# Performance work log

Hardware: AMD Instinct MI355X
Metric: run time of the kernel (lower is better)

The kernel has to match this reference:

```python
import jax, jax.numpy as jnp
import numpy as np

X = 2048      # hidden units per layer
Z = 4         # number of hidden layers
IN = 512      # input_dim
OUT = 256     # output_dim
B = 64        # batch
T = 128       # time steps
KEEP = 0.7    # Bernoulli keep prob y
RES = [0, 0, 1, 2]  # residual_in (first two unused by the branch structure)
NFUN = 5      # number of candidate transfer functions


def setup_inputs() -> dict:
    key = jax.random.key(0)
    ks = jax.random.split(key, 12)
    f32 = jnp.float32
    x = jax.random.normal(ks[0], (B, T, IN), f32)
    W_in = jax.random.normal(ks[1], (X, IN), f32) * jax.random.bernoulli(ks[2], KEEP, (X, IN)).astype(f32)
    b_in = jax.random.normal(ks[3], (X,), f32)
    W_h = jax.random.normal(ks[4], (Z, X, 2 * X), f32)
    # lateral inhibition block: hidden layer 1, second-half columns, zero diagonal
    lat = jax.random.normal(ks[5], (X, X), f32) * (1.0 - jnp.eye(X, dtype=f32))
    W_h = W_h.at[1, :, X:].set(lat)
    W_h = W_h * jax.random.bernoulli(ks[6], KEEP, (Z, X, 2 * X)).astype(f32)
    b_h = jax.random.normal(ks[7], (Z, X), f32)
    W_out = jax.random.normal(ks[8], (OUT, X), f32) * jax.random.bernoulli(ks[9], KEEP, (OUT, X)).astype(f32)
    b_out = jax.random.normal(ks[10], (OUT,), f32)
    act_ids = jax.random.randint(ks[11], (Z + 1, X), 0, NFUN)
    out_act_ids = jax.random.randint(jax.random.fold_in(key, 99), (OUT,), 0, NFUN)
    return dict(x=x, W_in=W_in, b_in=b_in, W_h=W_h, b_h=b_h,
                W_out=W_out, b_out=b_out, act_ids=act_ids, out_act_ids=out_act_ids)


def _rand_act(h, ids):
    # per-column random nonlinearity: ids [D] in {relu, sigmoid, tanh, leaky_relu(0.1), selu}
    stk = jnp.stack([
        jax.nn.relu(h),
        jax.nn.sigmoid(h),
        jnp.tanh(h),
        jnp.where(h >= 0, h, 0.1 * h),
        jax.nn.selu(h),
    ], axis=0)  # [5, B, D]
    oh = jax.nn.one_hot(ids, NFUN, dtype=h.dtype)  # [D, 5]
    return jnp.einsum('fbd,df->bd', stk, oh)


def _l2norm(v, eps=1e-12):
    # torch F.normalize along dim=1
    return v / jnp.maximum(jnp.linalg.norm(v, axis=1, keepdims=True), eps)


def reference(x, W_in, b_in, W_h, b_h, W_out, b_out, act_ids, out_act_ids):
    batch = x.shape[0]

    def step(carry, xt):
        bp, li = carry  # backprojection state, lateral inhibition state
        h0 = _rand_act(xt @ W_in.T + b_in, act_ids[0])
        h1 = _rand_act(jnp.concatenate([h0, bp], axis=-1) @ W_h[0].T + b_h[0], act_ids[1])
        h2 = _rand_act(jnp.concatenate([h1, li], axis=-1) @ W_h[1].T + b_h[1], act_ids[2])
        li_new = _l2norm(h2)
        outs = [h0, h1, h2]
        for i in range(2, Z):
            hin = jnp.concatenate([outs[i], outs[RES[i]]], axis=-1)
            outs.append(_rand_act(hin @ W_h[i].T + b_h[i], act_ids[i + 1]))
        bp_new = _l2norm(outs[-1])
        yt = _rand_act(outs[-1] @ W_out.T + b_out, out_act_ids)
        return (bp_new, li_new), yt

    init = (jnp.zeros((batch, X), x.dtype), jnp.zeros((batch, X), x.dtype))
    _, ys = jax.lax.scan(step, init, jnp.swapaxes(x, 0, 1))  # scan over time
    return jnp.swapaxes(ys, 0, 1)  # [B, T, OUT]
```

## Files before the change

### kernel.cpp

```cpp
#include <hip/hip_runtime.h>
#include <stdint.h>


typedef __bf16 bf16;
typedef __attribute__((ext_vector_type(8))) __bf16 bf16x8;
typedef __attribute__((ext_vector_type(4))) float f32x4;

#define BATCH 64
#define TSTEPS 128
#define INDIM 512
#define XDIM 2048
#define OUTDIM 256
#define SLOTE ((size_t)BATCH * XDIM)

__device__ __forceinline__ float apply_act(float h, int id) {
  switch (id) {
    case 0: return fmaxf(h, 0.0f);
    case 1: return 1.0f / (1.0f + __expf(-h));
    case 2: return tanhf(h);
    case 3: return h >= 0.0f ? h : 0.1f * h;
    default: {
      const float sc = 1.0507009873554805f;
      const float al = 1.6732632423543772f;
      return h > 0.0f ? sc * h : sc * al * (__expf(h) - 1.0f);
    }
  }
}

template <bool SCALE_A2, bool EMIT_SS>
__global__ __launch_bounds__(512, 2) void step_gemm8(
    const bf16* __restrict__ A1, const bf16* __restrict__ A2,
    const bf16* __restrict__ W, const float* __restrict__ bias,
    const int* __restrict__ acts, const float* __restrict__ ss_in,
    float* __restrict__ ss_out, bf16* __restrict__ outb) {
  const int tid = threadIdx.x;
  const int lane = tid & 63;
  const int w = tid >> 6;
  const int l15 = lane & 15;
  const int kb8 = (lane >> 4) * 8;
  const int nblk = blockIdx.x * 16;
  const int mrow = blockIdx.y * 32;

  const bf16* As = (w >= 4) ? A2 : A1;
  const int koff = (w & 3) * 512;
  const int wk = w * 512;

  const bf16* ap0 = As + (size_t)(mrow + l15) * 2048 + koff + kb8;
  const bf16* ap1 = ap0 + 16 * 2048;
  const bf16* bpw = W + (size_t)(nblk + l15) * 4096 + wk + kb8;

  f32x4 acc0 = {0.f, 0.f, 0.f, 0.f};
  f32x4 acc1 = {0.f, 0.f, 0.f, 0.f};
#pragma unroll
  for (int k = 0; k < 512; k += 32) {
    bf16x8 a0 = *(const bf16x8*)(ap0 + k);
    bf16x8 a1 = *(const bf16x8*)(ap1 + k);
    bf16x8 b  = *(const bf16x8*)(bpw + k);
    acc0 = __builtin_amdgcn_mfma_f32_16x16x32_bf16(a0, b, acc0, 0, 0, 0);
    acc1 = __builtin_amdgcn_mfma_f32_16x16x32_bf16(a1, b, acc1, 0, 0, 0);
  }

  __shared__ float red[8][32][17];
  const int q4 = lane >> 4;
#pragma unroll
  for (int r = 0; r < 4; r++) red[w][q4 * 4 + r][l15] = acc0[r];
#pragma unroll
  for (int r = 0; r < 4; r++) red[w][16 + q4 * 4 + r][l15] = acc1[r];
  __syncthreads();

  if (tid < 256) {
    const int row = tid >> 3;
    const int c0 = (tid & 7) * 2;
    const int rg = mrow + row;

    float scale = 1.0f;
    if (SCALE_A2) scale = 1.0f / fmaxf(sqrtf(ss_in[rg]), 1e-12f);

    float v[2];
#pragma unroll
    for (int j = 0; j < 2; j++) {
      int c = c0 + j;
      float lo = red[0][row][c] + red[1][row][c] + red[2][row][c] + red[3][row][c];
      float hi = red[4][row][c] + red[5][row][c] + red[6][row][c] + red[7][row][c];
      float pre = (SCALE_A2 ? (lo + scale * hi) : (lo + hi)) + bias[nblk + c];
      v[j] = apply_act(pre, acts[nblk + c]);
    }
    if (EMIT_SS) {
      float ss = v[0] * v[0] + v[1] * v[1];
      ss += __shfl_xor(ss, 1);
      ss += __shfl_xor(ss, 2);
      ss += __shfl_xor(ss, 4);
      if ((tid & 7) == 0) atomicAdd(ss_out + rg, ss);
    }
    union { bf16 b2[2]; uint32_t u; } pk;
    pk.b2[0] = (bf16)v[0];
    pk.b2[1] = (bf16)v[1];
    *(uint32_t*)(outb + (size_t)rg * XDIM + nblk + c0) = pk.u;
  }
}

__global__ __launch_bounds__(256) void h0_gemm(
    const bf16* __restrict__ A, const bf16* __restrict__ W,
    const float* __restrict__ bias, const int* __restrict__ acts,
    bf16* __restrict__ outp) {
  const int tid = threadIdx.x;
  const int lane = tid & 63;
  const int wv = tid >> 6;
  const int wm = (wv & 1) * 32;
  const int wn = (wv >> 1) * 64;
  const int nblk = blockIdx.x * 128;
  const int mblk = blockIdx.y * 64;
  const int l15 = lane & 15;
  const int kb8 = (lane >> 4) * 8;

  f32x4 acc[2][4];
  const f32x4 zero = {0.f, 0.f, 0.f, 0.f};
#pragma unroll
  for (int i = 0; i < 2; i++)
#pragma unroll
    for (int j = 0; j < 4; j++) acc[i][j] = zero;

  for (int kt = 0; kt < INDIM; kt += 32) {
    bf16x8 a[2], b[4];
#pragma unroll
    for (int mt = 0; mt < 2; mt++) {
      int m = mblk + wm + mt * 16 + l15;
      a[mt] = *(const bf16x8*)(A + (size_t)m * INDIM + kt + kb8);
    }
#pragma unroll
    for (int nt = 0; nt < 4; nt++) {
      int n = nblk + wn + nt * 16 + l15;
      b[nt] = *(const bf16x8*)(W + (size_t)n * INDIM + kt + kb8);
    }
#pragma unroll
    for (int mt = 0; mt < 2; mt++)
#pragma unroll
      for (int nt = 0; nt < 4; nt++)
        acc[mt][nt] = __builtin_amdgcn_mfma_f32_16x16x32_bf16(a[mt], b[nt], acc[mt][nt], 0, 0, 0);
  }

#pragma unroll
  for (int mt = 0; mt < 2; mt++) {
#pragma unroll
    for (int nt = 0; nt < 4; nt++) {
      int n = nblk + wn + nt * 16 + l15;
      float bv = bias[n];
      int aid = acts[n];
#pragma unroll
      for (int rr = 0; rr < 4; rr++) {
        int m = wm + mt * 16 + (lane >> 4) * 4 + rr;
        float v = apply_act(acc[mt][nt][rr] + bv, aid);
        int rowg = mblk + m;
        int bb = rowg >> 7;
        int tt = rowg & 127;
        outp[((size_t)tt * BATCH + bb) * XDIM + n] = (bf16)v;
      }
    }
  }
}

__global__ __launch_bounds__(256) void ybat_gemm(
    const bf16* __restrict__ extra, const bf16* __restrict__ h0,
    const bf16* __restrict__ Wout, const float* __restrict__ bout,
    const int* __restrict__ oact, float* __restrict__ out) {
  const int t = blockIdx.y;
  const int s = t + 1;
  const bf16* A = (s < 2) ? (extra + (size_t)s * SLOTE)
                          : (h0 + (size_t)(s - 2) * SLOTE);
  const int tid = threadIdx.x;
  const int lane = tid & 63;
  const int wv = tid >> 6;
  const int wm = (wv & 1) * 32;
  const int wn = (wv >> 1) * 64;
  const int nblk = blockIdx.x * 128;
  const int l15 = lane & 15;
  const int kb8 = (lane >> 4) * 8;

  f32x4 acc[2][4];
  const f32x4 zero = {0.f, 0.f, 0.f, 0.f};
#pragma unroll
  for (int i = 0; i < 2; i++)
#pragma unroll
    for (int j = 0; j < 4; j++) acc[i][j] = zero;

  for (int kt = 0; kt < XDIM; kt += 32) {
    bf16x8 a[2], b[4];
#pragma unroll
    for (int mt = 0; mt < 2; mt++) {
      int m = wm + mt * 16 + l15;
      a[mt] = *(const bf16x8*)(A + (size_t)m * XDIM + kt + kb8);
    }
#pragma unroll
    for (int nt = 0; nt < 4; nt++) {
      int n = nblk + wn + nt * 16 + l15;
      b[nt] = *(const bf16x8*)(Wout + (size_t)n * XDIM + kt + kb8);
    }
#pragma unroll
    for (int mt = 0; mt < 2; mt++)
#pragma unroll
      for (int nt = 0; nt < 4; nt++)
        acc[mt][nt] = __builtin_amdgcn_mfma_f32_16x16x32_bf16(a[mt], b[nt], acc[mt][nt], 0, 0, 0);
  }

#pragma unroll
  for (int mt = 0; mt < 2; mt++) {
#pragma unroll
    for (int nt = 0; nt < 4; nt++) {
      int n = nblk + wn + nt * 16 + l15;
      float bv = bout[n];
      int aid = oact[n];
#pragma unroll
      for (int rr = 0; rr < 4; rr++) {
        int b = wm + mt * 16 + (lane >> 4) * 4 + rr;
        float v = apply_act(acc[mt][nt][rr] + bv, aid);
        out[((size_t)b * TSTEPS + t) * OUTDIM + n] = v;
      }
    }
  }
}

__global__ __launch_bounds__(256) void cvt_bf16(
    const float* __restrict__ in, bf16* __restrict__ out, int n4) {
  int i = blockIdx.x * 256 + threadIdx.x;
  if (i < n4) {
    float4 v = ((const float4*)in)[i];
    union { bf16 b[4]; unsigned long long u; } pk;
    pk.b[0] = (bf16)v.x;
    pk.b[1] = (bf16)v.y;
    pk.b[2] = (bf16)v.z;
    pk.b[3] = (bf16)v.w;
    ((unsigned long long*)out)[i] = pk.u;
  }
}

__global__ __launch_bounds__(256) void zero32(uint32_t* __restrict__ p, int n) {
  int i = blockIdx.x * 256 + threadIdx.x;
  if (i < n) p[i] = 0u;
}

extern "C" void kernel_launch(void* const* d_in, const int* in_sizes, int n_in,
                              void* d_out, int out_size, void* d_ws, size_t ws_size,
                              hipStream_t stream) {
  const float* x     = (const float*)d_in[0];
  const float* W_in  = (const float*)d_in[1];
  const float* b_in  = (const float*)d_in[2];
  const float* W_h   = (const float*)d_in[3];
  const float* b_h   = (const float*)d_in[4];
  const float* W_out = (const float*)d_in[5];
  const float* b_out = (const float*)d_in[6];
  const int* act_ids = (const int*)d_in[7];
  const int* out_act = (const int*)d_in[8];
  float* out = (float*)d_out;

  char* w = (char*)d_ws;
  bf16* xbf   = (bf16*)w; w += (size_t)BATCH * TSTEPS * INDIM * 2;
  bf16* winb  = (bf16*)w; w += (size_t)XDIM * INDIM * 2;
  bf16* whb   = (bf16*)w; w += (size_t)4 * XDIM * (2 * XDIM) * 2;
  bf16* woutb = (bf16*)w; w += (size_t)OUTDIM * XDIM * 2;
  bf16* h0    = (bf16*)w; w += (size_t)TSTEPS * SLOTE * 2;
  bf16* h1    = (bf16*)w; w += SLOTE * 2;
  bf16* h3    = (bf16*)w; w += SLOTE * 2;
  char* zstart = w;
  bf16* extra = (bf16*)w; w += 2 * SLOTE * 2;
  bf16* h2a   = (bf16*)w; w += SLOTE * 2;
  bf16* h2b   = (bf16*)w; w += SLOTE * 2;
  float* ss_li = (float*)w; w += (size_t)(TSTEPS + 1) * BATCH * 4;
  float* ss_bp = (float*)w; w += (size_t)(TSTEPS + 1) * BATCH * 4;
  int zero_u32 = (int)((w - zstart) / 4);

  cvt_bf16<<<4096, 256, 0, stream>>>(x, xbf, (BATCH * TSTEPS * INDIM) / 4);
  cvt_bf16<<<1024, 256, 0, stream>>>(W_in, winb, (XDIM * INDIM) / 4);
  cvt_bf16<<<32768, 256, 0, stream>>>(W_h, whb, (4 * XDIM * 2 * XDIM) / 4);
  cvt_bf16<<<512, 256, 0, stream>>>(W_out, woutb, (OUTDIM * XDIM) / 4);
  zero32<<<(zero_u32 + 255) / 256, 256, 0, stream>>>((uint32_t*)zstart, zero_u32);
  h0_gemm<<<dim3(16, 128), 256, 0, stream>>>(xbf, winb, b_in, act_ids, h0);

  auto slotp = [&](int s) -> bf16* {
    return (s < 2) ? (extra + (size_t)s * SLOTE) : (h0 + (size_t)(s - 2) * SLOTE);
  };

  const size_t wstr = (size_t)XDIM * 2 * XDIM;
  for (int t = 0; t < TSTEPS; t++) {
    bf16* h2n = (t & 1) ? h2b : h2a;
    bf16* h2o = (t & 1) ? h2a : h2b;

    step_gemm8<true, false><<<dim3(128, 2), 512, 0, stream>>>(
        h0 + (size_t)t * SLOTE, slotp(t), whb, b_h, act_ids + XDIM,
        ss_bp + t * BATCH, nullptr, h1);
    step_gemm8<true, true><<<dim3(128, 2), 512, 0, stream>>>(
        h1, h2o, whb + wstr, b_h + XDIM, act_ids + 2 * XDIM,
        ss_li + t * BATCH, ss_li + (t + 1) * BATCH, h2n);
    step_gemm8<false, false><<<dim3(128, 2), 512, 0, stream>>>(
        h2n, h1, whb + 2 * wstr, b_h + 2 * XDIM, act_ids + 3 * XDIM,
        nullptr, nullptr, h3);
    step_gemm8<false, true><<<dim3(128, 2), 512, 0, stream>>>(
        h3, h2n, whb + 3 * wstr, b_h + 3 * XDIM, act_ids + 4 * XDIM,
        nullptr, ss_bp + (t + 1) * BATCH, slotp(t + 1));
  }

  ybat_gemm<<<dim3(2, TSTEPS), 256, 0, stream>>>(
      extra, h0, woutb, b_out, out_act, out);
}
```

Before: 8.865 ms.

## Fuse per-step layer launches into one persistent cooperative kernel with grid barriers

Replaces the 512 separate layer GEMM launches (4 per time step) with a single cooperative persistent kernel of 256 blocks. It loops over time and separates layers with an atomic-counter grid barrier. This removes per-launch overhead and inter-kernel gaps, which are large relative to each small GEMM. In exchange it depends on all blocks being co-resident and on correct fence semantics, and the spin barrier adds its own latency.

```diff
diff --git a/kernel.cpp b/kernel.cpp
--- a/kernel.cpp
+++ b/kernel.cpp
@@ -12,6 +12,7 @@
 #define XDIM 2048
 #define OUTDIM 256
 #define SLOTE ((size_t)BATCH * XDIM)
+#define NBLOCKS 256
 
 __device__ __forceinline__ float apply_act(float h, int id) {
   switch (id) {
@@ -27,19 +28,31 @@
   }
 }
 
+__device__ __forceinline__ void grid_sync(unsigned* bar, unsigned target) {
+  __syncthreads();
+  if (threadIdx.x == 0) {
+    __builtin_amdgcn_fence(__ATOMIC_RELEASE, "agent");
+    __hip_atomic_fetch_add(bar, 1u, __ATOMIC_RELAXED, __HIP_MEMORY_SCOPE_AGENT);
+    while (__hip_atomic_load(bar, __ATOMIC_RELAXED, __HIP_MEMORY_SCOPE_AGENT) < target) {
+      __builtin_amdgcn_s_sleep(1);
+    }
+    __builtin_amdgcn_fence(__ATOMIC_ACQUIRE, "agent");
+  }
+  __syncthreads();
+}
+
 template <bool SCALE_A2, bool EMIT_SS>
-__global__ __launch_bounds__(512, 2) void step_gemm8(
+__device__ __forceinline__ void layer_gemm(
+    const int tid, const int nblk, const int mrow,
     const bf16* __restrict__ A1, const bf16* __restrict__ A2,
     const bf16* __restrict__ W, const float* __restrict__ bias,
     const int* __restrict__ acts, const float* __restrict__ ss_in,
-    float* __restrict__ ss_out, bf16* __restrict__ outb) {
-  const int tid = threadIdx.x;
+    float* __restrict__ ss_out, bf16* __restrict__ outb,
+    float (&red)[8][32][17]) {
   const int lane = tid & 63;
   const int w = tid >> 6;
   const int l15 = lane & 15;
   const int kb8 = (lane >> 4) * 8;
-  const int nblk = blockIdx.x * 16;
-  const int mrow = blockIdx.y * 32;
 
   const bf16* As = (w >= 4) ? A2 : A1;
   const int koff = (w & 3) * 512;
@@ -60,7 +73,6 @@
     acc1 = __builtin_amdgcn_mfma_f32_16x16x32_bf16(a1, b, acc1, 0, 0, 0);
   }
 
-  __shared__ float red[8][32][17];
   const int q4 = lane >> 4;
 #pragma unroll
   for (int r = 0; r < 4; r++) red[w][q4 * 4 + r][l15] = acc0[r];
@@ -96,6 +108,61 @@
     pk.b2[0] = (bf16)v[0];
     pk.b2[1] = (bf16)v[1];
     *(uint32_t*)(outb + (size_t)rg * XDIM + nblk + c0) = pk.u;
+  }
+}
+
+struct StepParams {
+  bf16* h0;
+  bf16* extra;
+  bf16* h1;
+  bf16* h2a;
+  bf16* h2b;
+  bf16* h3;
+  const bf16* whb;
+  const float* b_h;
+  const int* acts;
+  float* ss_li;
+  float* ss_bp;
+  unsigned* bar;
+};
+
+__global__ __launch_bounds__(512, 2) void step_loop(StepParams p) {
+  __shared__ float red[8][32][17];
+  const int tid = threadIdx.x;
+  const int bid = blockIdx.x;
+  const int nblk = (bid & 127) * 16;
+  const int mrow = (bid >> 7) * 32;
+  const size_t wstr = (size_t)XDIM * 2 * XDIM;
+  unsigned tgt = 0;
+
+  for (int t = 0; t < TSTEPS; t++) {
+    const bf16* h4t = (t < 2) ? p.extra + (size_t)t * SLOTE
+                              : p.h0 + (size_t)(t - 2) * SLOTE;
+    bf16* h4n = (t + 1 < 2) ? p.extra + (size_t)(t + 1) * SLOTE
+                            : p.h0 + (size_t)(t - 1) * SLOTE;
+    bf16* h2n = (t & 1) ? p.h2b : p.h2a;
+    const bf16* h2o = (t & 1) ? p.h2a : p.h2b;
+
+    layer_gemm<true, false>(tid, nblk, mrow, p.h0 + (size_t)t * SLOTE, h4t,
+                            p.whb, p.b_h, p.acts + XDIM, p.ss_bp + t * BATCH,
+                            nullptr, p.h1, red);
+    tgt += NBLOCKS; grid_sync(p.bar, tgt);
+
+    layer_gemm<true, true>(tid, nblk, mrow, p.h1, h2o, p.whb + wstr,
+                           p.b_h + XDIM, p.acts + 2 * XDIM,
+                           p.ss_li + t * BATCH, p.ss_li + (t + 1) * BATCH,
+                           h2n, red);
+    tgt += NBLOCKS; grid_sync(p.bar, tgt);
+
+    layer_gemm<false, false>(tid, nblk, mrow, h2n, p.h1, p.whb + 2 * wstr,
+                             p.b_h + 2 * XDIM, p.acts + 3 * XDIM, nullptr,
+                             nullptr, p.h3, red);
+    tgt += NBLOCKS; grid_sync(p.bar, tgt);
+
+    layer_gemm<false, true>(tid, nblk, mrow, p.h3, h2n, p.whb + 3 * wstr,
+                            p.b_h + 3 * XDIM, p.acts + 4 * XDIM, nullptr,
+                            p.ss_bp + (t + 1) * BATCH, h4n, red);
+    tgt += NBLOCKS; grid_sync(p.bar, tgt);
   }
 }
 
@@ -266,6 +333,7 @@
   bf16* h2b   = (bf16*)w; w += SLOTE * 2;
   float* ss_li = (float*)w; w += (size_t)(TSTEPS + 1) * BATCH * 4;
   float* ss_bp = (float*)w; w += (size_t)(TSTEPS + 1) * BATCH * 4;
+  unsigned* bar = (unsigned*)w; w += 256;
   int zero_u32 = (int)((w - zstart) / 4);
 
   cvt_bf16<<<4096, 256, 0, stream>>>(x, xbf, (BATCH * TSTEPS * INDIM) / 4);
@@ -275,28 +343,22 @@
   zero32<<<(zero_u32 + 255) / 256, 256, 0, stream>>>((uint32_t*)zstart, zero_u32);
   h0_gemm<<<dim3(16, 128), 256, 0, stream>>>(xbf, winb, b_in, act_ids, h0);
 
-  auto slotp = [&](int s) -> bf16* {
-    return (s < 2) ? (extra + (size_t)s * SLOTE) : (h0 + (size_t)(s - 2) * SLOTE);
-  };
-
-  const size_t wstr = (size_t)XDIM * 2 * XDIM;
-  for (int t = 0; t < TSTEPS; t++) {
-    bf16* h2n = (t & 1) ? h2b : h2a;
-    bf16* h2o = (t & 1) ? h2a : h2b;
-
-    step_gemm8<true, false><<<dim3(128, 2), 512, 0, stream>>>(
-        h0 + (size_t)t * SLOTE, slotp(t), whb, b_h, act_ids + XDIM,
-        ss_bp + t * BATCH, nullptr, h1);
-    step_gemm8<true, true><<<dim3(128, 2), 512, 0, stream>>>(
-        h1, h2o, whb + wstr, b_h + XDIM, act_ids + 2 * XDIM,
-        ss_li + t * BATCH, ss_li + (t + 1) * BATCH, h2n);
-    step_gemm8<false, false><<<dim3(128, 2), 512, 0, stream>>>(
-        h2n, h1, whb + 2 * wstr, b_h + 2 * XDIM, act_ids + 3 * XDIM,
-        nullptr, nullptr, h3);
-    step_gemm8<false, true><<<dim3(128, 2), 512, 0, stream>>>(
-        h3, h2n, whb + 3 * wstr, b_h + 3 * XDIM, act_ids + 4 * XDIM,
-        nullptr, ss_bp + (t + 1) * BATCH, slotp(t + 1));
-  }
+  StepParams sp;
+  sp.h0 = h0;
+  sp.extra = extra;
+  sp.h1 = h1;
+  sp.h2a = h2a;
+  sp.h2b = h2b;
+  sp.h3 = h3;
+  sp.whb = whb;
+  sp.b_h = b_h;
+  sp.acts = act_ids;
+  sp.ss_li = ss_li;
+  sp.ss_bp = ss_bp;
+  sp.bar = bar;
+  void* kp[] = {&sp};
+  (void)hipLaunchCooperativeKernel((const void*)step_loop, dim3(NBLOCKS),
+                                   dim3(512), kp, 0, stream);
 
   ybat_gemm<<<dim3(2, TSTEPS), 256, 0, stream>>>(
       extra, h0, woutb, b_out, out_act, out);
```

After: 13.72 ms. 54.8% more time.
